# Kernel optimization log

Measured on AMD Instinct MI355X. Metric: run time of the kernel, lower is better.

## Reference

```python
import jax, jax.numpy as jnp
import numpy as np

NUM_FIELDS = 32  # m
EMBED = 64       # d
HIDDEN = 256     # conv output channels per layer


def setup_inputs() -> dict:
    key = jax.random.key(0)
    ks = jax.random.split(key, 8)
    m, d, H = NUM_FIELDS, EMBED, HIDDEN
    prev = [m, H // 2, H // 2]  # prev_dim entering each layer (split_half)
    x = jax.random.normal(ks[0], (1024, m, d), dtype=jnp.float32)
    W0 = jax.random.normal(ks[1], (m * prev[0], H), dtype=jnp.float32) * 0.02
    W1 = jax.random.normal(ks[2], (m * prev[1], H), dtype=jnp.float32) * 0.02
    W2 = jax.random.normal(ks[3], (m * prev[2], H), dtype=jnp.float32) * 0.02
    b0 = jnp.zeros((H,), jnp.float32)
    b1 = jnp.zeros((H,), jnp.float32)
    b2 = jnp.zeros((H,), jnp.float32)
    fc_in = H // 2 + H // 2 + H  # 512
    fc_W = jax.random.normal(ks[4], (fc_in, 1), dtype=jnp.float32) * 0.02
    fc_b = jnp.zeros((1,), jnp.float32)
    return {"x": x, "W0": W0, "b0": b0, "W1": W1, "b1": b1,
            "W2": W2, "b2": b2, "fc_W": fc_W, "fc_b": fc_b}


def _cin_forward(x, Ws, bs, fc_W, fc_b):
    num_layers = len(Ws)
    x0 = x  # (b, m, d)
    h = x
    xs = []
    for i in range(num_layers):
        b_, m, d = x0.shape
        n = h.shape[1]
        # outer product interaction: (b, m, n, d) -> flatten field pairs
        z = jnp.einsum('bmd,bnd->bmnd', x0, h).reshape(b_, m * n, d)
        # 1x1 Conv1D over channel dim (m*n): (b, k, d),(k, H) -> (b, H, d)
        y = jax.nn.relu(jnp.einsum('bkd,kh->bhd', z, Ws[i]) + bs[i][None, :, None])
        if i != num_layers - 1:  # split_half
            half = y.shape[1] // 2
            xcur, h = y[:, :half], y[:, half:]
        else:
            xcur = y
            h = y
        xs.append(xcur)
    f = jnp.concatenate(xs, axis=1)  # (b, fc_in, d)
    f = jnp.sum(f, axis=2)           # (b, fc_in)
    return f @ fc_W + fc_b           # (b, 1)


def reference(x, W0, b0, W1, b1, W2, b2, fc_W, fc_b):
    return _cin_forward(x, [W0, W1, W2], [b0, b1, b2], fc_W, fc_b)
```

## Files before the change

### kernel.cpp

```cpp
#include <hip/hip_runtime.h>

typedef __attribute__((ext_vector_type(8))) short bf16x8;
typedef __attribute__((ext_vector_type(4))) float f32x4;

__device__ __forceinline__ float bf2f(unsigned short u){
    unsigned int v = ((unsigned int)u) << 16;
    return __builtin_bit_cast(float, v);
}
__device__ __forceinline__ unsigned short f2bf(float f){
    unsigned int u = __builtin_bit_cast(unsigned int, f);
    u += 0x7FFFu + ((u >> 16) & 1u);
    return (unsigned short)(u >> 16);
}
__device__ __forceinline__ unsigned int cvt_pk_bf16(float lo, float hi){
    unsigned int r;
    asm("v_cvt_pk_bf16_f32 %0, %1, %2" : "=v"(r) : "v"(lo), "v"(hi));
    return r;
}
__device__ __forceinline__ unsigned int mulpack(unsigned int u, float xf){
    float flo = __builtin_bit_cast(float, u << 16);
    float fhi = __builtin_bit_cast(float, u & 0xffff0000u);
    return cvt_pk_bf16(xf * flo, xf * fhi);
}

__global__ void prep_wt(const float* __restrict__ W, unsigned short* __restrict__ Wt, int K){
    __shared__ float tile[64][65];
    const int k0 = blockIdx.x * 64;
    const int j0 = blockIdx.y * 64;
    const int t  = threadIdx.x;
    #pragma unroll
    for (int it = 0; it < 16; it++){
        int idx = it * 256 + t;
        int kr = idx >> 6, jc = idx & 63;
        tile[kr][jc] = W[(size_t)(k0 + kr) * 256 + j0 + jc];
    }
    __syncthreads();
    #pragma unroll
    for (int it = 0; it < 2; it++){
        int idx = it * 256 + t;
        int jr = idx >> 3, kc = (idx & 7) << 3;
        uint4 tv;
        unsigned short* ts = (unsigned short*)&tv;
        #pragma unroll
        for (int q = 0; q < 8; q++)
            ts[q] = f2bf(tile[kc + q][jr]);
        *(uint4*)(Wt + (size_t)(j0 + jr) * K + k0 + kc) = tv;
    }
}

__global__ void prep_x(const float* __restrict__ x, unsigned short* __restrict__ Xt){
    int b = blockIdx.x;
    int t = threadIdx.x;
    #pragma unroll
    for (int it = 0; it < 8; it++){
        int o = it * 256 + t;
        int d = o >> 5, m = o & 31;
        Xt[(size_t)b * 2048 + o] = f2bf(x[(size_t)b * 2048 + m * 64 + d]);
    }
}

__global__ void init_out(float* __restrict__ out, const float* __restrict__ fcb){
    int i = blockIdx.x * 256 + threadIdx.x;
    if (i < 1024) out[i] = fcb[0];
}

template<int NN, int KTOT, int JX, bool HAS_HOUT>
__global__ __launch_bounds__(256, 2) void cin_stage(
    const unsigned short* __restrict__ Xt,
    const unsigned short* __restrict__ Hin,
    const unsigned short* __restrict__ Wt,
    const float* __restrict__ bias,
    const float* __restrict__ fcW,
    unsigned short* __restrict__ Hout,
    float* __restrict__ out)
{
    constexpr int SB  = NN / 32;
    constexpr int XS  = 40;
    constexpr int ZS  = (NN == 32) ? 40 : 136;
    constexpr int XLSZ = 128 * XS;
    constexpr int HLSZ = (NN == 32) ? 0 : 128 * ZS;
    constexpr int ZMSZ = 128 * ZS;
    constexpr int NEED = XLSZ + HLSZ + ZMSZ;
    constexpr int SMSZ = NEED > 17408 ? NEED : 17408;

    __shared__ unsigned short smem[SMSZ];
    unsigned short* const Xl = smem;
    unsigned short* const Hl = (NN == 32) ? smem : (smem + XLSZ);
    unsigned short* const Zm = smem + XLSZ + HLSZ;
    unsigned short* const Yl = smem;

    const int t    = threadIdx.x;
    const int lane = t & 63;
    const int w    = t >> 6;
    const int li   = lane & 15;
    const int lq   = lane >> 4;
    const int bpair = blockIdx.x;

    {
        const int c  = t >> 1;
        const int b  = bpair * 2 + (c >> 6);
        const int d  = c & 63;
        const int half = t & 1;
        const int mh = half << 4;
        const uint4* xsrc = (const uint4*)(Xt + ((size_t)b << 11) + (d << 5) + mh);
        uint4 x0 = xsrc[0], x1 = xsrc[1];
        *(uint4*)(Xl + c * XS + mh)     = x0;
        *(uint4*)(Xl + c * XS + mh + 8) = x1;
        if (NN == 128){
            const int nh = half << 6;
            const uint4* hsrc = (const uint4*)(Hin + (size_t)((b << 6) + d) * 128 + nh);
            #pragma unroll
            for (int q = 0; q < 8; q++){
                uint4 hv = hsrc[q];
                *(uint4*)(Hl + c * ZS + nh + q * 8) = hv;
            }
        }
    }

    const int bc = t & 127;
    const int bh = t >> 7;
    constexpr int CPT = (NN == 128) ? 8 : 2;
    auto build = [&](int m){
        float xf = bf2f(Xl[bc * XS + m]);
        #pragma unroll
        for (int j = 0; j < CPT; j++){
            int off = (bh * CPT + j) << 3;
            uint4 hv = *(const uint4*)(Hl + bc * ZS + off);
            uint4 zv;
            zv.x = mulpack(hv.x, xf);
            zv.y = mulpack(hv.y, xf);
            zv.z = mulpack(hv.z, xf);
            zv.w = mulpack(hv.w, xf);
            *(uint4*)(Zm + bc * ZS + off) = zv;
        }
    };

    const unsigned short* wrow = Wt + (size_t)((w << 6) + li) * KTOT + (lq << 3);
    bf16x8 A[4][SB];
    auto aload = [&](int m){
        #pragma unroll
        for (int jt = 0; jt < 4; jt++)
            #pragma unroll
            for (int s = 0; s < SB; s++)
                A[jt][s] = *(const bf16x8*)(wrow + (size_t)jt * 16 * KTOT + (m * SB + s) * 32);
    };

    f32x4 acc[4][8];
    #pragma unroll
    for (int jt = 0; jt < 4; jt++)
        #pragma unroll
        for (int ct = 0; ct < 8; ct++)
            acc[jt][ct] = (f32x4){0.f, 0.f, 0.f, 0.f};

    __syncthreads();
    build(0);
    aload(0);
    __syncthreads();

    for (int m = 0; m < 32; m++){
        #pragma unroll
        for (int s = 0; s < SB; s++){
            bf16x8 Bf[8];
            #pragma unroll
            for (int ct = 0; ct < 8; ct++)
                Bf[ct] = *(const bf16x8*)(Zm + ((ct << 4) + li) * ZS + (s << 5) + (lq << 3));
            #pragma unroll
            for (int ct = 0; ct < 8; ct++)
                #pragma unroll
                for (int jt = 0; jt < 4; jt++)
                    acc[jt][ct] = __builtin_amdgcn_mfma_f32_16x16x32_bf16(
                        A[jt][s], Bf[ct], acc[jt][ct], 0, 0, 0);
        }
        __syncthreads();
        if (m < 31){
            aload(m + 1);
            build(m + 1);
        }
        __syncthreads();
    }

    if (HAS_HOUT) __syncthreads();

    float pfc0 = 0.f, pfc1 = 0.f;
    #pragma unroll
    for (int jt = 0; jt < 4; jt++){
        const int jb = (w << 6) + (jt << 4) + (lq << 2);
        float bv[4], fv[4];
        #pragma unroll
        for (int r = 0; r < 4; r++){
            int j = jb + r;
            bv[r] = bias[j];
            fv[r] = (j < JX) ? fcW[j] : 0.f;
        }
        #pragma unroll
        for (int ct = 0; ct < 8; ct++){
            f32x4 f = acc[jt][ct];
            int c = (ct << 4) + li;
            float ps = 0.f;
            #pragma unroll
            for (int r = 0; r < 4; r++){
                float y = f[r] + bv[r];
                y = y > 0.f ? y : 0.f;
                ps += fv[r] * y;
                if (HAS_HOUT){
                    int j = jb + r;
                    if (j >= 128)
                        Yl[(j - 128) * 136 + c] = f2bf(y);
                }
            }
            if (ct < 4) pfc0 += ps; else pfc1 += ps;
        }
    }
    #pragma unroll
    for (int off = 32; off; off >>= 1){
        pfc0 += __shfl_xor(pfc0, off, 64);
        pfc1 += __shfl_xor(pfc1, off, 64);
    }
    if (lane == 0){
        atomicAdd(out + bpair * 2 + 0, pfc0);
        atomicAdd(out + bpair * 2 + 1, pfc1);
    }

    if (HAS_HOUT){
        __syncthreads();
        const int c  = t >> 1;
        const int nh = (t & 1) << 6;
        unsigned short* gdst = Hout + (size_t)(bpair * 128 + c) * 128 + nh;
        #pragma unroll
        for (int i8 = 0; i8 < 8; i8++){
            uint4 tv;
            unsigned short* tmp2 = (unsigned short*)&tv;
            #pragma unroll
            for (int q = 0; q < 8; q++)
                tmp2[q] = Yl[(nh + i8 * 8 + q) * 136 + c];
            *(uint4*)(gdst + i8 * 8) = tv;
        }
    }
}

extern "C" void kernel_launch(void* const* d_in, const int* in_sizes, int n_in,
                              void* d_out, int out_size, void* d_ws, size_t ws_size,
                              hipStream_t stream){
    const float* x   = (const float*)d_in[0];
    const float* W0  = (const float*)d_in[1];
    const float* b0  = (const float*)d_in[2];
    const float* W1  = (const float*)d_in[3];
    const float* b1  = (const float*)d_in[4];
    const float* W2  = (const float*)d_in[5];
    const float* b2  = (const float*)d_in[6];
    const float* fcW = (const float*)d_in[7];
    const float* fcb = (const float*)d_in[8];
    float* out = (float*)d_out;

    char* ws = (char*)d_ws;
    unsigned short* Xt  = (unsigned short*)(ws);
    unsigned short* Wt0 = (unsigned short*)(ws + 4194304);
    unsigned short* Wt1 = (unsigned short*)(ws + 4718592);
    unsigned short* Wt2 = (unsigned short*)(ws + 6815744);
    unsigned short* H0  = (unsigned short*)(ws + 8912896);
    unsigned short* H1  = (unsigned short*)(ws + 25690112);

    prep_wt<<<dim3(16, 4), 256, 0, stream>>>(W0, Wt0, 1024);
    prep_wt<<<dim3(64, 4), 256, 0, stream>>>(W1, Wt1, 4096);
    prep_wt<<<dim3(64, 4), 256, 0, stream>>>(W2, Wt2, 4096);
    prep_x <<<1024, 256, 0, stream>>>(x, Xt);
    init_out<<<4, 256, 0, stream>>>(out, fcb);

    cin_stage< 32, 1024, 128, true ><<<512, 256, 0, stream>>>(Xt, Xt, Wt0, b0, fcW,       H0, out);
    cin_stage<128, 4096, 128, true ><<<512, 256, 0, stream>>>(Xt, H0, Wt1, b1, fcW + 128, H1, out);
    cin_stage<128, 4096, 256, false><<<512, 256, 0, stream>>>(Xt, H1, Wt2, b2, fcW + 256, nullptr, out);
}
```

Before: 402.2 us.

## Double-buffer interaction tile and prefetch weights per k-step to overlap with MFMA

The z-tile build for field m+1 is interleaved with the MFMA loop for field m by using two LDS buffers (Zm0/Zm1). The H slice is kept in registers instead of LDS, and the x tile is stored transposed. Weight fragments are double-buffered per 32-wide k-step instead of being loaded for a whole field at once. This cuts one barrier per field and hides global and LDS latency behind matrix math, at the cost of more LDS (two Z buffers), more registers for hreg, and a possible occupancy drop.

After: 586.6 us. 1.46x slower.

```diff
diff --git a/kernel.cpp b/kernel.cpp
--- a/kernel.cpp
+++ b/kernel.cpp
@@ -63,6 +63,49 @@
     int i = blockIdx.x * 256 + threadIdx.x;
     if (i < 1024) out[i] = fcb[0];
 }
+
+#define CIN_MBODY(MM, P)                                                        \
+    {                                                                           \
+        unsigned short* const Zr = ((MM) & 1) ? Zm1 : Zm0;                      \
+        unsigned short* const Zw = ((MM) & 1) ? Zm0 : Zm1;                      \
+        const int mnext = (MM) + 1;                                             \
+        float xf = 0.f;                                                         \
+        if (mnext < 32) xf = bf2f(Xlt[mnext * XTS + bc]);                       \
+        _Pragma("unroll")                                                       \
+        for (int s = 0; s < SB; s++){                                           \
+            const int ktn = (MM) * SB + s + 1;                                  \
+            if (ktn < KT){                                                      \
+                _Pragma("unroll")                                               \
+                for (int jt = 0; jt < 4; jt++)                                  \
+                    A2[((P) + s + 1) & 1][jt] =                                 \
+                        *(const bf16x8*)(wrow + (size_t)jt * 16 * KTOT + ktn * 32); \
+            }                                                                   \
+            bf16x8 Bf[8];                                                       \
+            _Pragma("unroll")                                                   \
+            for (int ct = 0; ct < 8; ct++)                                      \
+                Bf[ct] = *(const bf16x8*)(Zr + ((ct << 4) + li) * ZS + (s << 5) + (lq << 3)); \
+            _Pragma("unroll")                                                   \
+            for (int ct = 0; ct < 8; ct++)                                      \
+                _Pragma("unroll")                                               \
+                for (int jt = 0; jt < 4; jt++)                                  \
+                    acc[jt][ct] = __builtin_amdgcn_mfma_f32_16x16x32_bf16(      \
+                        A2[((P) + s) & 1][jt], Bf[ct], acc[jt][ct], 0, 0, 0);   \
+            if (mnext < 32){                                                    \
+                _Pragma("unroll")                                               \
+                for (int q = 0; q < CPS; q++){                                  \
+                    const int c8 = s * CPS + q;                                 \
+                    uint4 hv = hreg[c8];                                        \
+                    uint4 zv;                                                   \
+                    zv.x = mulpack(hv.x, xf);                                   \
+                    zv.y = mulpack(hv.y, xf);                                   \
+                    zv.z = mulpack(hv.z, xf);                                   \
+                    zv.w = mulpack(hv.w, xf);                                   \
+                    *(uint4*)(Zw + bc * ZS + ((bh * CPT + c8) << 3)) = zv;      \
+                }                                                               \
+            }                                                                   \
+        }                                                                       \
+        __syncthreads();                                                        \
+    }
 
 template<int NN, int KTOT, int JX, bool HAS_HOUT>
 __global__ __launch_bounds__(256, 2) void cin_stage(
@@ -75,75 +118,80 @@
     float* __restrict__ out)
 {
     constexpr int SB  = NN / 32;
-    constexpr int XS  = 40;
+    constexpr int KT  = KTOT / 32;
+    constexpr int CPT = NN / 16;
+    constexpr int CPS = CPT / SB;
+    constexpr int XTS = 136;
     constexpr int ZS  = (NN == 32) ? 40 : 136;
-    constexpr int XLSZ = 128 * XS;
-    constexpr int HLSZ = (NN == 32) ? 0 : 128 * ZS;
+    constexpr int XTSZ = 32 * XTS;
     constexpr int ZMSZ = 128 * ZS;
-    constexpr int NEED = XLSZ + HLSZ + ZMSZ;
+    constexpr int NEED = XTSZ + 2 * ZMSZ;
     constexpr int SMSZ = NEED > 17408 ? NEED : 17408;
 
     __shared__ unsigned short smem[SMSZ];
-    unsigned short* const Xl = smem;
-    unsigned short* const Hl = (NN == 32) ? smem : (smem + XLSZ);
-    unsigned short* const Zm = smem + XLSZ + HLSZ;
-    unsigned short* const Yl = smem;
+    unsigned short* const Xlt = smem;
+    unsigned short* const Zm0 = smem + XTSZ;
+    unsigned short* const Zm1 = Zm0 + ZMSZ;
+    unsigned short* const Yl  = smem;
 
     const int t    = threadIdx.x;
     const int lane = t & 63;
     const int w    = t >> 6;
     const int li   = lane & 15;
     const int lq   = lane >> 4;
+    const int bc   = t & 127;
+    const int bh   = t >> 7;
     const int bpair = blockIdx.x;
 
     {
         const int c  = t >> 1;
         const int b  = bpair * 2 + (c >> 6);
         const int d  = c & 63;
-        const int half = t & 1;
-        const int mh = half << 4;
+        const int mh = (t & 1) << 4;
         const uint4* xsrc = (const uint4*)(Xt + ((size_t)b << 11) + (d << 5) + mh);
         uint4 x0 = xsrc[0], x1 = xsrc[1];
-        *(uint4*)(Xl + c * XS + mh)     = x0;
-        *(uint4*)(Xl + c * XS + mh + 8) = x1;
+        const unsigned short* xs0 = (const unsigned short*)&x0;
+        const unsigned short* xs1 = (const unsigned short*)&x1;
+        #pragma unroll
+        for (int q = 0; q < 8; q++) Xlt[(mh + q) * XTS + c]     = xs0[q];
+        #pragma unroll
+        for (int q = 0; q < 8; q++) Xlt[(mh + 8 + q) * XTS + c] = xs1[q];
+    }
+    uint4 hreg[CPT];
+    {
+        const int b = bpair * 2 + (bc >> 6);
+        const int d = bc & 63;
         if (NN == 128){
-            const int nh = half << 6;
-            const uint4* hsrc = (const uint4*)(Hin + (size_t)((b << 6) + d) * 128 + nh);
-            #pragma unroll
-            for (int q = 0; q < 8; q++){
-                uint4 hv = hsrc[q];
-                *(uint4*)(Hl + c * ZS + nh + q * 8) = hv;
-            }
-        }
-    }
-
-    const int bc = t & 127;
-    const int bh = t >> 7;
-    constexpr int CPT = (NN == 128) ? 8 : 2;
-    auto build = [&](int m){
-        float xf = bf2f(Xl[bc * XS + m]);
-        #pragma unroll
-        for (int j = 0; j < CPT; j++){
-            int off = (bh * CPT + j) << 3;
-            uint4 hv = *(const uint4*)(Hl + bc * ZS + off);
+            const uint4* hsrc = (const uint4*)(Hin + (size_t)((b << 6) + d) * 128 + (bh << 6));
+            #pragma unroll
+            for (int q = 0; q < CPT; q++) hreg[q] = hsrc[q];
+        } else {
+            const uint4* hsrc = (const uint4*)(Xt + ((size_t)b << 11) + (d << 5) + (bh << 4));
+            #pragma unroll
+            for (int q = 0; q < CPT; q++) hreg[q] = hsrc[q];
+        }
+    }
+    __syncthreads();
+
+    {
+        float xf = bf2f(Xlt[bc]);
+        #pragma unroll
+        for (int c8 = 0; c8 < CPT; c8++){
+            uint4 hv = hreg[c8];
             uint4 zv;
             zv.x = mulpack(hv.x, xf);
             zv.y = mulpack(hv.y, xf);
             zv.z = mulpack(hv.z, xf);
             zv.w = mulpack(hv.w, xf);
-            *(uint4*)(Zm + bc * ZS + off) = zv;
-        }
-    };
+            *(uint4*)(Zm0 + bc * ZS + ((bh * CPT + c8) << 3)) = zv;
+        }
+    }
 
     const unsigned short* wrow = Wt + (size_t)((w << 6) + li) * KTOT + (lq << 3);
-    bf16x8 A[4][SB];
-    auto aload = [&](int m){
-        #pragma unroll
-        for (int jt = 0; jt < 4; jt++)
-            #pragma unroll
-            for (int s = 0; s < SB; s++)
-                A[jt][s] = *(const bf16x8*)(wrow + (size_t)jt * 16 * KTOT + (m * SB + s) * 32);
-    };
+    bf16x8 A2[2][4];
+    #pragma unroll
+    for (int jt = 0; jt < 4; jt++)
+        A2[0][jt] = *(const bf16x8*)(wrow + (size_t)jt * 16 * KTOT);
 
     f32x4 acc[4][8];
     #pragma unroll
@@ -153,33 +201,11 @@
             acc[jt][ct] = (f32x4){0.f, 0.f, 0.f, 0.f};
 
     __syncthreads();
-    build(0);
-    aload(0);
-    __syncthreads();
-
-    for (int m = 0; m < 32; m++){
-        #pragma unroll
-        for (int s = 0; s < SB; s++){
-            bf16x8 Bf[8];
-            #pragma unroll
-            for (int ct = 0; ct < 8; ct++)
-                Bf[ct] = *(const bf16x8*)(Zm + ((ct << 4) + li) * ZS + (s << 5) + (lq << 3));
-            #pragma unroll
-            for (int ct = 0; ct < 8; ct++)
-                #pragma unroll
-                for (int jt = 0; jt < 4; jt++)
-                    acc[jt][ct] = __builtin_amdgcn_mfma_f32_16x16x32_bf16(
-                        A[jt][s], Bf[ct], acc[jt][ct], 0, 0, 0);
-        }
-        __syncthreads();
-        if (m < 31){
-            aload(m + 1);
-            build(m + 1);
-        }
-        __syncthreads();
-    }
-
-    if (HAS_HOUT) __syncthreads();
+
+    for (int m = 0; m < 32; m += 2){
+        CIN_MBODY(m, 0);
+        CIN_MBODY(m + 1, (SB & 1));
+    }
 
     float pfc0 = 0.f, pfc1 = 0.f;
     #pragma unroll
```

## Retile waves to 128x64 output tiles with double-buffered weight fragment prefetch

Applied to the files above, without the earlier changes.

Changes the per-wave output tiling from 64 output channels x 128 columns to 128 channels x 64 columns, with waves split into a channel group and a column group. Weight fragments are now loaded one K-step ahead into a two-slot register buffer, instead of being loaded all at once between the barriers. The loop is unrolled by two m-steps so the buffer parity stays static. The goal is to hide global weight-load latency behind the MFMAs and to cut LDS B-fragment reads per MFMA. In exchange each wave reloads more weight fragments and uses more registers, which may hurt occupancy.

After: 689.1 us. +71.3%, slower.

```diff
diff --git a/kernel.cpp b/kernel.cpp
--- a/kernel.cpp
+++ b/kernel.cpp
@@ -63,6 +63,34 @@
     int i = blockIdx.x * 256 + threadIdx.x;
     if (i < 1024) out[i] = fcb[0];
 }
+
+#define CIN_MBODY(MM, P)                                                         \
+    {                                                                            \
+        const int mnext = (MM) + 1;                                              \
+        _Pragma("unroll")                                                        \
+        for (int s = 0; s < SB; s++){                                            \
+            const int ktn = (MM) * SB + s + 1;                                   \
+            if (ktn < KT){                                                       \
+                _Pragma("unroll")                                                \
+                for (int jt = 0; jt < 8; jt++)                                   \
+                    A2[((P) + s + 1) & 1][jt] =                                  \
+                        *(const bf16x8*)(wrow + (size_t)jt * 16 * KTOT + ktn * 32); \
+            }                                                                    \
+            bf16x8 Bf[4];                                                        \
+            _Pragma("unroll")                                                    \
+            for (int ct = 0; ct < 4; ct++)                                       \
+                Bf[ct] = *(const bf16x8*)(Zm + (cgo + (ct << 4) + li) * ZS + (s << 5) + (lq << 3)); \
+            _Pragma("unroll")                                                    \
+            for (int ct = 0; ct < 4; ct++)                                       \
+                _Pragma("unroll")                                                 \
+                for (int jt = 0; jt < 8; jt++)                                   \
+                    acc[jt][ct] = __builtin_amdgcn_mfma_f32_16x16x32_bf16(       \
+                        A2[((P) + s) & 1][jt], Bf[ct], acc[jt][ct], 0, 0, 0);    \
+        }                                                                        \
+        __syncthreads();                           \
+        if (mnext < 32) build(mnext);                                            \
+        __syncthreads();                                    \
+    }
 
 template<int NN, int KTOT, int JX, bool HAS_HOUT>
 __global__ __launch_bounds__(256, 2) void cin_stage(
@@ -75,8 +103,9 @@
     float* __restrict__ out)
 {
     constexpr int SB  = NN / 32;
+    constexpr int KT  = KTOT / 32;
     constexpr int XS  = 40;
-    constexpr int ZS  = (NN == 32) ? 40 : 136;
+    constexpr int ZS  = (NN == 32) ? XS : 136;
     constexpr int XLSZ = 128 * XS;
     constexpr int HLSZ = (NN == 32) ? 0 : 128 * ZS;
     constexpr int ZMSZ = 128 * ZS;
@@ -92,8 +121,11 @@
     const int t    = threadIdx.x;
     const int lane = t & 63;
     const int w    = t >> 6;
+    const int jg   = w & 1;
+    const int cg   = w >> 1;
     const int li   = lane & 15;
     const int lq   = lane >> 4;
+    const int cgo  = cg << 6;
     const int bpair = blockIdx.x;
 
     {
@@ -135,56 +167,32 @@
         }
     };
 
-    const unsigned short* wrow = Wt + (size_t)((w << 6) + li) * KTOT + (lq << 3);
-    bf16x8 A[4][SB];
-    auto aload = [&](int m){
-        #pragma unroll
-        for (int jt = 0; jt < 4; jt++)
-            #pragma unroll
-            for (int s = 0; s < SB; s++)
-                A[jt][s] = *(const bf16x8*)(wrow + (size_t)jt * 16 * KTOT + (m * SB + s) * 32);
-    };
-
-    f32x4 acc[4][8];
-    #pragma unroll
-    for (int jt = 0; jt < 4; jt++)
-        #pragma unroll
-        for (int ct = 0; ct < 8; ct++)
+    const unsigned short* wrow = Wt + (size_t)((jg << 7) + li) * KTOT + (lq << 3);
+    bf16x8 A2[2][8];
+    #pragma unroll
+    for (int jt = 0; jt < 8; jt++)
+        A2[0][jt] = *(const bf16x8*)(wrow + (size_t)jt * 16 * KTOT);
+
+    f32x4 acc[8][4];
+    #pragma unroll
+    for (int jt = 0; jt < 8; jt++)
+        #pragma unroll
+        for (int ct = 0; ct < 4; ct++)
             acc[jt][ct] = (f32x4){0.f, 0.f, 0.f, 0.f};
 
     __syncthreads();
     build(0);
-    aload(0);
     __syncthreads();
 
-    for (int m = 0; m < 32; m++){
-        #pragma unroll
-        for (int s = 0; s < SB; s++){
-            bf16x8 Bf[8];
-            #pragma unroll
-            for (int ct = 0; ct < 8; ct++)
-                Bf[ct] = *(const bf16x8*)(Zm + ((ct << 4) + li) * ZS + (s << 5) + (lq << 3));
-            #pragma unroll
-            for (int ct = 0; ct < 8; ct++)
-                #pragma unroll
-                for (int jt = 0; jt < 4; jt++)
-                    acc[jt][ct] = __builtin_amdgcn_mfma_f32_16x16x32_bf16(
-                        A[jt][s], Bf[ct], acc[jt][ct], 0, 0, 0);
-        }
-        __syncthreads();
-        if (m < 31){
-            aload(m + 1);
-            build(m + 1);
-        }
-        __syncthreads();
-    }
-
-    if (HAS_HOUT) __syncthreads();
-
-    float pfc0 = 0.f, pfc1 = 0.f;
-    #pragma unroll
-    for (int jt = 0; jt < 4; jt++){
-        const int jb = (w << 6) + (jt << 4) + (lq << 2);
+    for (int m = 0; m < 32; m += 2){
+        CIN_MBODY(m, 0);
+        CIN_MBODY(m + 1, (SB & 1));
+    }
+
+    float pfc = 0.f;
+    #pragma unroll
+    for (int jt = 0; jt < 8; jt++){
+        const int jb = (jg << 7) + (jt << 4) + (lq << 2);
         float bv[4], fv[4];
         #pragma unroll
         for (int r = 0; r < 4; r++){
@@ -193,33 +201,27 @@
             fv[r] = (j < JX) ? fcW[j] : 0.f;
         }
         #pragma unroll
-        for (int ct = 0; ct < 8; ct++){
+        for (int ct = 0; ct < 4; ct++){
             f32x4 f = acc[jt][ct];
-            int c = (ct << 4) + li;
-            float ps = 0.f;
+            int c = cgo + (ct << 4) + li;
             #pragma unroll
             for (int r = 0; r < 4; r++){
                 float y = f[r] + bv[r];
                 y = y > 0.f ? y : 0.f;
-                ps += fv[r] * y;
+                pfc += fv[r] * y;
                 if (HAS_HOUT){
                     int j = jb + r;
                     if (j >= 128)
                         Yl[(j - 128) * 136 + c] = f2bf(y);
                 }
             }
-            if (ct < 4) pfc0 += ps; else pfc1 += ps;
-        }
-    }
-    #pragma unroll
-    for (int off = 32; off; off >>= 1){
-        pfc0 += __shfl_xor(pfc0, off, 64);
-        pfc1 += __shfl_xor(pfc1, off, 64);
-    }
-    if (lane == 0){
-        atomicAdd(out + bpair * 2 + 0, pfc0);
-        atomicAdd(out + bpair * 2 + 1, pfc1);
-    }
+        }
+    }
+    #pragma unroll
+    for (int off = 32; off; off >>= 1)
+        pfc += __shfl_xor(pfc, off, 64);
+    if (lane == 0)
+        atomicAdd(out + bpair * 2 + cg, pfc);
 
     if (HAS_HOUT){
         __syncthreads();
```
